# Optimization experiments

Measured on AMD Instinct MI355X. Metric: run time of the kernel, lower is better.

The kernel has to match this reference:

```python
import jax, jax.numpy as jnp
import numpy as np

HEADS = 16


def setup_inputs() -> dict:
    key0 = jax.random.key(0)
    ks = jax.random.split(key0, 12)
    B, S, H = 4, 2048, 1024
    init = lambda k, shape: (jax.random.normal(k, shape, dtype=jnp.float32) * 0.02)
    return {
        "key": jax.random.normal(ks[0], (B, S, H), dtype=jnp.float32),
        "query": jax.random.normal(ks[1], (B, S, H), dtype=jnp.float32),
        "value": jax.random.normal(ks[2], (B, S, H), dtype=jnp.float32),
        "mask": jnp.zeros((B, 1, S, S), dtype=jnp.float32),  # additive mask
        "wq": init(ks[3], (H, H)), "bq": jnp.zeros((H,), jnp.float32),
        "wk": init(ks[4], (H, H)), "bk": jnp.zeros((H,), jnp.float32),
        "wv": init(ks[5], (H, H)), "bv": jnp.zeros((H,), jnp.float32),
        "wo": init(ks[6], (H, H)), "bo": jnp.zeros((H,), jnp.float32),
    }


def reference(key, query, value, mask, wq, bq, wk, bk, wv, bv, wo, bo):
    B, S, H = query.shape
    Hs = H // HEADS
    # Linear projections (torch Linear: x @ W^T + b), split heads -> [B, Hn, S, Hs]
    split = lambda x: x.reshape(B, S, HEADS, Hs).transpose(0, 2, 1, 3)
    q = split(query @ wq.T + bq)
    k = split(key @ wk.T + bk)
    v = split(value @ wv.T + bv)
    scale = 1.0 / jnp.sqrt(jnp.asarray(Hs, q.dtype))
    scores = jnp.einsum("bhqd,bhkd->bhqk", q, k) * scale  # [B, Hn, S, S]
    probs = jax.nn.softmax(scores + mask, axis=-1)  # dropout p=0 -> identity
    ctx = jnp.einsum("bhqk,bhkd->bhqd", probs, v)
    ctx = ctx.transpose(0, 2, 1, 3).reshape(B, S, H)
    return ctx @ wo.T + bo
```

## Files before the change

kernel.cpp:

```cpp
#include <hip/hip_runtime.h>
#include <hip/hip_bf16.h>

typedef __bf16 bf16;
typedef __bf16 bf16x4 __attribute__((ext_vector_type(4)));
typedef __bf16 bf16x8 __attribute__((ext_vector_type(8)));
typedef float f32x4 __attribute__((ext_vector_type(4)));

#define MFMA16(a, b, c) __builtin_amdgcn_mfma_f32_16x16x32_bf16((a), (b), (c), 0, 0, 0)

__device__ __forceinline__ int xcd_swizzle(int bid, int nblk) {
  const int per = nblk >> 3;
  return (bid & 7) * per + (bid >> 3);
}

__device__ __forceinline__ void gload_lds16(const bf16* g, bf16* lds) {
  __builtin_amdgcn_global_load_lds(
      (const __attribute__((address_space(1))) void*)g,
      (__attribute__((address_space(3))) void*)lds, 16, 0, 0);
}

template <typename T> struct StageRegs;
template <> struct StageRegs<float> { float4 lo[4], hi[4]; };
template <> struct StageRegs<bf16> { bf16x8 v[4]; };

template <typename T>
__device__ __forceinline__ void stage_issue(StageRegs<T>& r, const T* base,
                                            int rowstride, int brc, int k0,
                                            int tid) {
#pragma unroll
  for (int i = 0; i < 4; ++i) {
    const int c = i * 256 + tid;
    const int row = c >> 3, lin = c & 7;
    const T* p = base + (size_t)(brc + row) * rowstride + k0 + lin * 8;
    if constexpr (sizeof(T) == 4) {
      r.lo[i] = *reinterpret_cast<const float4*>(p);
      r.hi[i] = *reinterpret_cast<const float4*>(p + 4);
    } else {
      r.v[i] = *reinterpret_cast<const bf16x8*>(p);
    }
  }
}

template <typename T>
__device__ __forceinline__ void stage_write(const StageRegs<T>& r, bf16* sm,
                                            int tid) {
#pragma unroll
  for (int i = 0; i < 4; ++i) {
    const int c = i * 256 + tid;
    const int row = c >> 3, lin = c & 7;
    const int slot = lin ^ (row & 7);
    bf16x8 v;
    if constexpr (sizeof(T) == 4) {
      const float4 a = r.lo[i], b = r.hi[i];
      v[0] = (bf16)a.x; v[1] = (bf16)a.y; v[2] = (bf16)a.z; v[3] = (bf16)a.w;
      v[4] = (bf16)b.x; v[5] = (bf16)b.y; v[6] = (bf16)b.z; v[7] = (bf16)b.w;
    } else {
      v = r.v[i];
    }
    *reinterpret_cast<bf16x8*>(sm + row * 64 + slot * 8) = v;
  }
}

template <typename TA, typename TB, typename TC>
__global__ __launch_bounds__(256, 2) void gemm_bias_kernel(
    const TA* __restrict__ A, const TB* __restrict__ W,
    const float* __restrict__ bias, TC* __restrict__ C, int M, int N, int K,
    int nbc, float cscale) {
  __shared__ bf16 Asm[2][128 * 64];
  __shared__ bf16 Bsm[2][128 * 64];
  const int tid = threadIdx.x;
  const int lane = tid & 63;
  const int wid = tid >> 6;
  const int l15 = lane & 15;
  const int l4 = lane >> 4;
  const int bid = xcd_swizzle(blockIdx.x, gridDim.x);
  const int brow = (bid / nbc) << 7;
  const int bcol = (bid % nbc) << 7;
  const int wm = (wid >> 1) << 6;
  const int wn = (wid & 1) << 6;

  f32x4 acc[4][4] = {};

  StageRegs<TA> ra;
  StageRegs<TB> rb;
  stage_issue(ra, A, K, brow, 0, tid);
  stage_issue(rb, W, K, bcol, 0, tid);

  const int nt = K >> 6;
  int p = 0;
  for (int t = 0; t < nt; ++t) {
    stage_write(ra, Asm[p], tid);
    stage_write(rb, Bsm[p], tid);
    if (t + 1 < nt) {
      stage_issue(ra, A, K, brow, (t + 1) << 6, tid);
      stage_issue(rb, W, K, bcol, (t + 1) << 6, tid);
    }
    __syncthreads();
#pragma unroll
    for (int kk = 0; kk < 2; ++kk) {
      bf16x8 af[4], bfr[4];
#pragma unroll
      for (int m = 0; m < 4; ++m) {
        const int row = wm + m * 16 + l15;
        const int slot = (kk * 4 + l4) ^ (row & 7);
        af[m] = *reinterpret_cast<const bf16x8*>(Asm[p] + row * 64 + slot * 8);
      }
#pragma unroll
      for (int n = 0; n < 4; ++n) {
        const int row = wn + n * 16 + l15;
        const int slot = (kk * 4 + l4) ^ (row & 7);
        bfr[n] = *reinterpret_cast<const bf16x8*>(Bsm[p] + row * 64 + slot * 8);
      }
      __builtin_amdgcn_s_setprio(1);
#pragma unroll
      for (int m = 0; m < 4; ++m)
#pragma unroll
        for (int n = 0; n < 4; ++n)
          acc[m][n] = MFMA16(af[m], bfr[n], acc[m][n]);
      __builtin_amdgcn_s_setprio(0);
    }
    p ^= 1;
  }

  const int r0 = brow + wm + l4 * 4;
  const int c0 = bcol + wn + l15;
#pragma unroll
  for (int n = 0; n < 4; ++n) {
    const float bv = bias[c0 + n * 16];
#pragma unroll
    for (int m = 0; m < 4; ++m) {
#pragma unroll
      for (int r = 0; r < 4; ++r) {
        C[(size_t)(r0 + m * 16 + r) * N + (c0 + n * 16)] =
            (TC)((acc[m][n][r] + bv) * cscale);
      }
    }
  }
}

__global__ __launch_bounds__(256) void transpose_v_kernel(
    const bf16* __restrict__ V, bf16* __restrict__ Vt) {
  __shared__ unsigned short t[64][72];
  const int bid = blockIdx.x;
  const int st = bid & 31;
  const int h = (bid >> 5) & 15;
  const int b = bid >> 9;
  const int s0 = st * 64;
  const int tid = threadIdx.x;
#pragma unroll
  for (int i = 0; i < 2; ++i) {
    const int c = i * 256 + tid;
    const int row = c >> 3;
    const int off = (c & 7) * 8;
    const uint4 v = *reinterpret_cast<const uint4*>(
        &V[(size_t)(b * 2048 + s0 + row) * 1024 + h * 64 + off]);
    *reinterpret_cast<uint4*>(&t[row][off]) = v;
  }
  __syncthreads();
#pragma unroll
  for (int i = 0; i < 2; ++i) {
    const int c = i * 256 + tid;
    const int d = c >> 3;
    const int so = (c & 7) * 8;
    unsigned short tmp[8] __attribute__((aligned(16)));
#pragma unroll
    for (int j = 0; j < 8; ++j) tmp[j] = t[so + j][d];
    *reinterpret_cast<uint4*>(
        &Vt[(size_t)((b * 16 + h) * 64 + d) * 2048 + s0 + so]) =
        *reinterpret_cast<const uint4*>(tmp);
  }
}

__global__ __launch_bounds__(256, 4) void attn_kernel(
    const bf16* __restrict__ Q, const bf16* __restrict__ Kt,
    const bf16* __restrict__ Vt, const float* __restrict__ mask,
    bf16* __restrict__ ctx) {
  __shared__ bf16 Ksm[2][64 * 64];
  __shared__ bf16 Vsm[2][64 * 64];
  __shared__ bf16 Pl[4][1024];
  const int lid = xcd_swizzle(blockIdx.x, 2048);
  const int h = lid & 15;
  const int qb = (lid >> 4) & 31;
  const int b = lid >> 9;
  const int tid = threadIdx.x;
  const int lane = tid & 63;
  const int wid = tid >> 6;
  const int l15 = lane & 15;
  const int l4 = lane >> 4;

  const int qbase = qb * 64 + wid * 16;

  bf16x8 qf[2];
#pragma unroll
  for (int kk = 0; kk < 2; ++kk)
    qf[kk] = *reinterpret_cast<const bf16x8*>(
        &Q[(size_t)(b * 2048 + qbase + l15) * 1024 + h * 64 + kk * 32 + l4 * 8]);

  f32x4 o[4] = {};
  float mrow = -1e30f, lrow = 0.f;

  const float LOG2E = 1.44269504088896f;
  const bf16* Kb = Kt + (size_t)b * 2048 * 1024 + h * 64;
  const bf16* Vb = Vt + (size_t)(b * 16 + h) * 64 * 2048;
  const float* Mb = mask + (size_t)b * 2048 * 2048;
  char* Pw = reinterpret_cast<char*>(&Pl[wid][0]);
  const int qsw = (l15 & 7);

  f32x4 mreg[4];

  auto stage = [&](int p, int k0) {
#pragma unroll
    for (int i = 0; i < 2; ++i) {
      const int c = i * 256 + tid;
      const int row = c >> 3;
      const int lin = (c & 7) ^ (row & 7);
      gload_lds16(Kb + (size_t)(k0 + row) * 1024 + lin * 8, &Ksm[p][c * 8]);
      gload_lds16(Vb + (size_t)row * 2048 + k0 + lin * 8, &Vsm[p][c * 8]);
    }
  };
  auto load_mask = [&](int k0) {
#pragma unroll
    for (int kt = 0; kt < 4; ++kt)
      mreg[kt] = *reinterpret_cast<const f32x4*>(
          &Mb[(size_t)(qbase + l15) * 2048 + k0 + kt * 16 + l4 * 4]);
  };

  stage(0, 0);
  load_mask(0);
  asm volatile("s_waitcnt vmcnt(0)" ::: "memory");
  __syncthreads();

  int p = 0;
  for (int t = 0; t < 32; ++t) {
    const int k0 = t << 6;
    if (t + 1 < 32) stage(p ^ 1, k0 + 64);

    f32x4 sf[4] = {};
    __builtin_amdgcn_s_setprio(1);
#pragma unroll
    for (int kt = 0; kt < 4; ++kt) {
#pragma unroll
      for (int kk = 0; kk < 2; ++kk) {
        const int row = kt * 16 + l15;
        const int slot = (kk * 4 + l4) ^ (row & 7);
        const bf16x8 kf =
            *reinterpret_cast<const bf16x8*>(&Ksm[p][row * 64 + slot * 8]);
        sf[kt] = MFMA16(kf, qf[kk], sf[kt]);
      }
    }
    __builtin_amdgcn_s_setprio(0);

    float rmax = -1e30f;
#pragma unroll
    for (int kt = 0; kt < 4; ++kt) {
#pragma unroll
      for (int r = 0; r < 4; ++r) {
        const float x = sf[kt][r] + mreg[kt][r];
        sf[kt][r] = x;
        rmax = fmaxf(rmax, x);
      }
    }
    if (t + 1 < 32) load_mask(k0 + 64);

    rmax = fmaxf(rmax, __shfl_xor(rmax, 16, 64));
    rmax = fmaxf(rmax, __shfl_xor(rmax, 32, 64));

    if (!__all(rmax <= mrow + 8.0f)) {
      const float mn = fmaxf(mrow, rmax);
      const float alpha = __builtin_exp2f((mrow - mn) * LOG2E);
      mrow = mn;
      lrow *= alpha;
      float ar[4];
#pragma unroll
      for (int r = 0; r < 4; ++r) ar[r] = __shfl(alpha, l4 * 4 + r, 64);
#pragma unroll
      for (int dt = 0; dt < 4; ++dt)
#pragma unroll
        for (int r = 0; r < 4; ++r) o[dt][r] *= ar[r];
    }

    const float negmL = -mrow * LOG2E;
    float rsum = 0.f;
#pragma unroll
    for (int kt = 0; kt < 4; ++kt) {
      bf16x4 pk;
#pragma unroll
      for (int r = 0; r < 4; ++r) {
        const float pv = __builtin_exp2f(__builtin_fmaf(sf[kt][r], LOG2E, negmL));
        rsum += pv;
        pk[r] = (bf16)pv;
      }
      const int slot = (kt * 4 + l4) ^ qsw;
      *reinterpret_cast<bf16x4*>(Pw + l15 * 128 + slot * 8) = pk;
    }
    rsum += __shfl_xor(rsum, 16, 64);
    rsum += __shfl_xor(rsum, 32, 64);
    lrow += rsum;

#pragma unroll
    for (int kk = 0; kk < 2; ++kk) {
      const int s0 = kk * 8 + l4 * 2;
      const bf16x4 plo =
          *reinterpret_cast<const bf16x4*>(Pw + l15 * 128 + (s0 ^ qsw) * 8);
      const bf16x4 phi =
          *reinterpret_cast<const bf16x4*>(Pw + l15 * 128 + ((s0 + 1) ^ qsw) * 8);
      bf16x8 pf;
#pragma unroll
      for (int j = 0; j < 4; ++j) { pf[j] = plo[j]; pf[j + 4] = phi[j]; }
      __builtin_amdgcn_s_setprio(1);
#pragma unroll
      for (int dt = 0; dt < 4; ++dt) {
        const int row = dt * 16 + l15;
        const int slot = (kk * 4 + l4) ^ (row & 7);
        const bf16x8 vf =
            *reinterpret_cast<const bf16x8*>(&Vsm[p][row * 64 + slot * 8]);
        o[dt] = MFMA16(pf, vf, o[dt]);
      }
      __builtin_amdgcn_s_setprio(0);
    }

    asm volatile("s_waitcnt vmcnt(0)" ::: "memory");
    __syncthreads();
    p ^= 1;
  }

  float linv[4];
#pragma unroll
  for (int r = 0; r < 4; ++r)
    linv[r] = __builtin_amdgcn_rcpf(__shfl(lrow, l4 * 4 + r, 64));
#pragma unroll
  for (int dt = 0; dt < 4; ++dt) {
#pragma unroll
    for (int r = 0; r < 4; ++r) {
      const int q = qbase + l4 * 4 + r;
      ctx[(size_t)(b * 2048 + q) * 1024 + h * 64 + dt * 16 + l15] =
          (bf16)(o[dt][r] * linv[r]);
    }
  }
}

extern "C" void kernel_launch(void* const* d_in, const int* in_sizes, int n_in,
                              void* d_out, int out_size, void* d_ws,
                              size_t ws_size, hipStream_t stream) {
  const float* key = (const float*)d_in[0];
  const float* query = (const float*)d_in[1];
  const float* value = (const float*)d_in[2];
  const float* mask = (const float*)d_in[3];
  const float* wq = (const float*)d_in[4];
  const float* bq = (const float*)d_in[5];
  const float* wk = (const float*)d_in[6];
  const float* bk = (const float*)d_in[7];
  const float* wv = (const float*)d_in[8];
  const float* bv = (const float*)d_in[9];
  const float* wo = (const float*)d_in[10];
  const float* bo = (const float*)d_in[11];
  float* out = (float*)d_out;

  const size_t NBSH = (size_t)4 * 2048 * 1024;
  bf16* Qws = (bf16*)d_ws;
  bf16* Kws = Qws + NBSH;
  bf16* Vt = Kws + NBSH;
  bf16* Vtmp = (bf16*)d_out;

  const dim3 blk(256);
  gemm_bias_kernel<float, float, bf16><<<512, blk, 0, stream>>>(
      query, wq, bq, Qws, 8192, 1024, 1024, 8, 0.125f);
  gemm_bias_kernel<float, float, bf16><<<512, blk, 0, stream>>>(
      key, wk, bk, Kws, 8192, 1024, 1024, 8, 1.0f);
  gemm_bias_kernel<float, float, bf16><<<512, blk, 0, stream>>>(
      value, wv, bv, Vtmp, 8192, 1024, 1024, 8, 1.0f);
  transpose_v_kernel<<<2048, blk, 0, stream>>>(Vtmp, Vt);
  attn_kernel<<<2048, blk, 0, stream>>>(Qws, Kws, Vt, mask, Qws);
  gemm_bias_kernel<bf16, float, float><<<512, blk, 0, stream>>>(
      Qws, wo, bo, out, 8192, 1024, 1024, 8, 1.0f);
}
```

Baseline: 323.0 us.

## Switch attention to 32x32x16 MFMA with 128-query blocks and register P exchange

```diff
diff --git a/kernel.cpp b/kernel.cpp
--- a/kernel.cpp
+++ b/kernel.cpp
@@ -2,11 +2,13 @@
 #include <hip/hip_bf16.h>
 
 typedef __bf16 bf16;
-typedef __bf16 bf16x4 __attribute__((ext_vector_type(4)));
 typedef __bf16 bf16x8 __attribute__((ext_vector_type(8)));
 typedef float f32x4 __attribute__((ext_vector_type(4)));
+typedef float f32x16 __attribute__((ext_vector_type(16)));
+typedef unsigned u32x4 __attribute__((ext_vector_type(4)));
 
 #define MFMA16(a, b, c) __builtin_amdgcn_mfma_f32_16x16x32_bf16((a), (b), (c), 0, 0, 0)
+#define MFMA32(a, b, c) __builtin_amdgcn_mfma_f32_32x32x16_bf16((a), (b), (c), 0, 0, 0)
 
 __device__ __forceinline__ int xcd_swizzle(int bid, int nblk) {
   const int per = nblk >> 3;
@@ -17,6 +19,12 @@
   __builtin_amdgcn_global_load_lds(
       (const __attribute__((address_space(1))) void*)g,
       (__attribute__((address_space(3))) void*)lds, 16, 0, 0);
+}
+
+__device__ __forceinline__ unsigned pack2bf(float a, float b) {
+  const unsigned short ua = __builtin_bit_cast(unsigned short, (bf16)a);
+  const unsigned short ub = __builtin_bit_cast(unsigned short, (bf16)b);
+  return (unsigned)ua | ((unsigned)ub << 16);
 }
 
 template <typename T> struct StageRegs;
@@ -171,42 +179,39 @@
   }
 }
 
-__global__ __launch_bounds__(256, 4) void attn_kernel(
+__global__ __launch_bounds__(256, 2) void attn_kernel(
     const bf16* __restrict__ Q, const bf16* __restrict__ Kt,
     const bf16* __restrict__ Vt, const float* __restrict__ mask,
     bf16* __restrict__ ctx) {
   __shared__ bf16 Ksm[2][64 * 64];
   __shared__ bf16 Vsm[2][64 * 64];
-  __shared__ bf16 Pl[4][1024];
-  const int lid = xcd_swizzle(blockIdx.x, 2048);
+  const int lid = xcd_swizzle(blockIdx.x, 1024);
   const int h = lid & 15;
-  const int qb = (lid >> 4) & 31;
-  const int b = lid >> 9;
+  const int qb = (lid >> 4) & 15;
+  const int b = lid >> 8;
   const int tid = threadIdx.x;
   const int lane = tid & 63;
   const int wid = tid >> 6;
-  const int l15 = lane & 15;
-  const int l4 = lane >> 4;
-
-  const int qbase = qb * 64 + wid * 16;
-
-  bf16x8 qf[2];
-#pragma unroll
-  for (int kk = 0; kk < 2; ++kk)
-    qf[kk] = *reinterpret_cast<const bf16x8*>(
-        &Q[(size_t)(b * 2048 + qbase + l15) * 1024 + h * 64 + kk * 32 + l4 * 8]);
-
-  f32x4 o[4] = {};
+  const int l31 = lane & 31;
+  const int h5 = lane >> 5;
+
+  const int qbase = qb * 128 + wid * 32;
+
+  bf16x8 qf[4];
+#pragma unroll
+  for (int c = 0; c < 4; ++c)
+    qf[c] = *reinterpret_cast<const bf16x8*>(
+        &Q[(size_t)(b * 2048 + qbase + l31) * 1024 + h * 64 + c * 16 + h5 * 8]);
+
+  f32x16 o[2] = {};
   float mrow = -1e30f, lrow = 0.f;
 
   const float LOG2E = 1.44269504088896f;
   const bf16* Kb = Kt + (size_t)b * 2048 * 1024 + h * 64;
   const bf16* Vb = Vt + (size_t)(b * 16 + h) * 64 * 2048;
   const float* Mb = mask + (size_t)b * 2048 * 2048;
-  char* Pw = reinterpret_cast<char*>(&Pl[wid][0]);
-  const int qsw = (l15 & 7);
-
-  f32x4 mreg[4];
+
+  f32x4 mreg[2][4];
 
   auto stage = [&](int p, int k0) {
 #pragma unroll
@@ -220,9 +225,11 @@
   };
   auto load_mask = [&](int k0) {
 #pragma unroll
-    for (int kt = 0; kt < 4; ++kt)
-      mreg[kt] = *reinterpret_cast<const f32x4*>(
-          &Mb[(size_t)(qbase + l15) * 2048 + k0 + kt * 16 + l4 * 4]);
+    for (int s = 0; s < 2; ++s)
+#pragma unroll
+      for (int g = 0; g < 4; ++g)
+        mreg[s][g] = *reinterpret_cast<const f32x4*>(
+            &Mb[(size_t)(qbase + l31) * 2048 + k0 + s * 32 + g * 8 + h5 * 4]);
   };
 
   stage(0, 0);
@@ -235,34 +242,33 @@
     const int k0 = t << 6;
     if (t + 1 < 32) stage(p ^ 1, k0 + 64);
 
-    f32x4 sf[4] = {};
+    f32x16 sf[2] = {};
     __builtin_amdgcn_s_setprio(1);
 #pragma unroll
-    for (int kt = 0; kt < 4; ++kt) {
-#pragma unroll
-      for (int kk = 0; kk < 2; ++kk) {
-        const int row = kt * 16 + l15;
-        const int slot = (kk * 4 + l4) ^ (row & 7);
+    for (int s = 0; s < 2; ++s) {
+#pragma unroll
+      for (int c = 0; c < 4; ++c) {
+        const int row = s * 32 + l31;
+        const int slot = (2 * c + h5) ^ (row & 7);
         const bf16x8 kf =
             *reinterpret_cast<const bf16x8*>(&Ksm[p][row * 64 + slot * 8]);
-        sf[kt] = MFMA16(kf, qf[kk], sf[kt]);
+        sf[s] = MFMA32(kf, qf[c], sf[s]);
       }
     }
     __builtin_amdgcn_s_setprio(0);
 
     float rmax = -1e30f;
 #pragma unroll
-    for (int kt = 0; kt < 4; ++kt) {
-#pragma unroll
-      for (int r = 0; r < 4; ++r) {
-        const float x = sf[kt][r] + mreg[kt][r];
-        sf[kt][r] = x;
+    for (int s = 0; s < 2; ++s) {
+#pragma unroll
+      for (int reg = 0; reg < 16; ++reg) {
+        const float x = sf[s][reg] + mreg[s][reg >> 2][reg & 3];
+        sf[s][reg] = x;
         rmax = fmaxf(rmax, x);
       }
     }
     if (t + 1 < 32) load_mask(k0 + 64);
 
-    rmax = fmaxf(rmax, __shfl_xor(rmax, 16, 64));
     rmax = fmaxf(rmax, __shfl_xor(rmax, 32, 64));
 
     if (!__all(rmax <= mrow + 8.0f)) {
@@ -270,51 +276,58 @@
       const float alpha = __builtin_exp2f((mrow - mn) * LOG2E);
       mrow = mn;
       lrow *= alpha;
-      float ar[4];
-#pragma unroll
-      for (int r = 0; r < 4; ++r) ar[r] = __shfl(alpha, l4 * 4 + r, 64);
-#pragma unroll
-      for (int dt = 0; dt < 4; ++dt)
-#pragma unroll
-        for (int r = 0; r < 4; ++r) o[dt][r] *= ar[r];
+#pragma unroll
+      for (int reg = 0; reg < 16; ++reg) {
+        const int qr = (reg & 3) + 8 * (reg >> 2) + 4 * h5;
+        const float a = __shfl(alpha, qr, 64);
+        o[0][reg] *= a;
+        o[1][reg] *= a;
+      }
     }
 
     const float negmL = -mrow * LOG2E;
     float rsum = 0.f;
-#pragma unroll
-    for (int kt = 0; kt < 4; ++kt) {
-      bf16x4 pk;
-#pragma unroll
-      for (int r = 0; r < 4; ++r) {
-        const float pv = __builtin_exp2f(__builtin_fmaf(sf[kt][r], LOG2E, negmL));
-        rsum += pv;
-        pk[r] = (bf16)pv;
-      }
-      const int slot = (kt * 4 + l4) ^ qsw;
-      *reinterpret_cast<bf16x4*>(Pw + l15 * 128 + slot * 8) = pk;
-    }
-    rsum += __shfl_xor(rsum, 16, 64);
+    unsigned pk[2][4][2];
+#pragma unroll
+    for (int s = 0; s < 2; ++s) {
+#pragma unroll
+      for (int g = 0; g < 4; ++g) {
+        float pv[4];
+#pragma unroll
+        for (int r = 0; r < 4; ++r) {
+          pv[r] = __builtin_exp2f(
+              __builtin_fmaf(sf[s][g * 4 + r], LOG2E, negmL));
+          rsum += pv[r];
+        }
+        pk[s][g][0] = pack2bf(pv[0], pv[1]);
+        pk[s][g][1] = pack2bf(pv[2], pv[3]);
+      }
+    }
     rsum += __shfl_xor(rsum, 32, 64);
     lrow += rsum;
 
 #pragma unroll
-    for (int kk = 0; kk < 2; ++kk) {
-      const int s0 = kk * 8 + l4 * 2;
-      const bf16x4 plo =
-          *reinterpret_cast<const bf16x4*>(Pw + l15 * 128 + (s0 ^ qsw) * 8);
-      const bf16x4 phi =
-          *reinterpret_cast<const bf16x4*>(Pw + l15 * 128 + ((s0 + 1) ^ qsw) * 8);
-      bf16x8 pf;
-#pragma unroll
-      for (int j = 0; j < 4; ++j) { pf[j] = plo[j]; pf[j + 4] = phi[j]; }
+    for (int c = 0; c < 4; ++c) {
+      const int s = c >> 1;
+      const int ge = (2 * c) & 3;
+      const int go = (2 * c + 1) & 3;
+      const unsigned send0 = h5 ? pk[s][ge][0] : pk[s][go][0];
+      const unsigned send1 = h5 ? pk[s][ge][1] : pk[s][go][1];
+      const unsigned recv0 = __shfl_xor(send0, 32, 64);
+      const unsigned recv1 = __shfl_xor(send1, 32, 64);
+      const unsigned own0 = h5 ? pk[s][go][0] : pk[s][ge][0];
+      const unsigned own1 = h5 ? pk[s][go][1] : pk[s][ge][1];
+      const u32x4 uu = {h5 ? recv0 : own0, h5 ? recv1 : own1,
+                        h5 ? own0 : recv0, h5 ? own1 : recv1};
+      const bf16x8 pa = __builtin_bit_cast(bf16x8, uu);
       __builtin_amdgcn_s_setprio(1);
 #pragma unroll
-      for (int dt = 0; dt < 4; ++dt) {
-        const int row = dt * 16 + l15;
-        const int slot = (kk * 4 + l4) ^ (row & 7);
+      for (int dsub = 0; dsub < 2; ++dsub) {
+        const int row = dsub * 32 + l31;
+        const int slot = (2 * c + h5) ^ (row & 7);
         const bf16x8 vf =
             *reinterpret_cast<const bf16x8*>(&Vsm[p][row * 64 + slot * 8]);
-        o[dt] = MFMA16(pf, vf, o[dt]);
+        o[dsub] = MFMA32(pa, vf, o[dsub]);
       }
       __builtin_amdgcn_s_setprio(0);
     }
@@ -324,17 +337,16 @@
     p ^= 1;
   }
 
-  float linv[4];
-#pragma unroll
-  for (int r = 0; r < 4; ++r)
-    linv[r] = __builtin_amdgcn_rcpf(__shfl(lrow, l4 * 4 + r, 64));
-#pragma unroll
-  for (int dt = 0; dt < 4; ++dt) {
-#pragma unroll
-    for (int r = 0; r < 4; ++r) {
-      const int q = qbase + l4 * 4 + r;
-      ctx[(size_t)(b * 2048 + q) * 1024 + h * 64 + dt * 16 + l15] =
-          (bf16)(o[dt][r] * linv[r]);
+  const float linv = __builtin_amdgcn_rcpf(lrow);
+#pragma unroll
+  for (int reg = 0; reg < 16; ++reg) {
+    const int qr = (reg & 3) + 8 * (reg >> 2) + 4 * h5;
+    const float li = __shfl(linv, qr, 64);
+    const int q = qbase + qr;
+#pragma unroll
+    for (int dsub = 0; dsub < 2; ++dsub) {
+      ctx[(size_t)(b * 2048 + q) * 1024 + h * 64 + dsub * 32 + l31] =
+          (bf16)(o[dsub][reg] * li);
     }
   }
 }
@@ -370,7 +382,7 @@
   gemm_bias_kernel<float, float, bf16><<<512, blk, 0, stream>>>(
       value, wv, bv, Vtmp, 8192, 1024, 1024, 8, 1.0f);
   transpose_v_kernel<<<2048, blk, 0, stream>>>(Vtmp, Vt);
-  attn_kernel<<<2048, blk, 0, stream>>>(Qws, Kws, Vt, mask, Qws);
+  attn_kernel<<<1024, blk, 0, stream>>>(Qws, Kws, Vt, mask, Qws);
   gemm_bias_kernel<bf16, float, float><<<512, blk, 0, stream>>>(
       Qws, wo, bo, out, 8192, 1024, 1024, 8, 1.0f);
 }
```

Result: no change. 327.1 us (+1.2%).
